# Performance work log

Hardware: AMD Instinct MI355X
Metric: run time of the kernel (lower is better)

The kernel has to match this reference:

```python
import jax, jax.numpy as jnp
import numpy as np

POOL = (7, 7)          # pool_size (Ph, Pw)
N_REGIONS = 32         # n_regions kept after IoU suppression
IOU_THR = 0.4          # IoU_threshold
B, R, H, W, C = 4, 160, 128, 128, 64


def _iou_matrix(boxes):
    # boxes: [R, 4] in (x, y, w, h); standard pairwise IoU
    x0, y0 = boxes[:, 0], boxes[:, 1]
    x1, y1 = x0 + boxes[:, 2], y0 + boxes[:, 3]
    xa = jnp.maximum(x0[:, None], x0[None, :])
    ya = jnp.maximum(y0[:, None], y0[None, :])
    xb = jnp.minimum(x1[:, None], x1[None, :])
    yb = jnp.minimum(y1[:, None], y1[None, :])
    inter = jnp.maximum(xb - xa, 0.0) * jnp.maximum(yb - ya, 0.0)
    area = boxes[:, 2] * boxes[:, 3]
    return inter / (area[:, None] + area[None, :] - inter)


def _nms_indices(boxes, thr, n_regions):
    # Greedy duplicate suppression in given (descending-objectness) order,
    # then first n_regions surviving indices, padded with the last index (R-1).
    r = boxes.shape[0]
    iou = _iou_matrix(boxes)
    ar = jnp.arange(r)

    def step(keep, i):
        sup = keep[i] & (iou[i] > thr) & (ar > i)
        return keep & ~sup, None

    keep, _ = jax.lax.scan(step, jnp.ones((r,), bool), jnp.arange(r - 1))
    rank = jnp.cumsum(keep) - 1                      # position among kept
    pos = jnp.where(keep, rank, n_regions)           # non-kept / overflow -> dropped
    idx = jnp.full((n_regions,), r - 1, dtype=jnp.int32)
    return idx.at[pos].set(ar.astype(jnp.int32), mode='drop')


def _fix_span(lo, hi, p, s):
    # enforce hi - lo >= p within [0, s], replicating clip_RoI's padding logic
    pad = p - (hi - lo)
    fmin = lo < pad // 2
    fmax = (s - hi) < (1 + pad) // 2
    sym = (pad > 0) & ~(fmin | fmax)
    lo2 = jnp.where(sym, lo - pad // 2, lo)
    hi2 = jnp.where(sym, hi + (1 + pad) // 2, hi)
    lo2 = jnp.where((pad > 0) & fmin, 0, lo2)
    hi2 = jnp.where((pad > 0) & fmin, p, hi2)
    lo2 = jnp.where((pad > 0) & fmax, s - p, lo2)
    hi2 = jnp.where((pad > 0) & fmax, s, hi2)
    return lo2, hi2


def _clip_rois(roi, h, w, ph, pw):
    x0 = jnp.maximum(0, roi[..., 0].astype(jnp.int32))
    y0 = jnp.maximum(0, roi[..., 1].astype(jnp.int32))
    x1 = jnp.minimum(w, (roi[..., 0] + roi[..., 2]).astype(jnp.int32))
    y1 = jnp.minimum(h, (roi[..., 1] + roi[..., 3]).astype(jnp.int32))
    x0, x1 = _fix_span(x0, x1, pw, w)
    y0, y1 = _fix_span(y0, y1, ph, h)
    return jnp.stack([x0, y0, x1 - x0, y1 - y0], axis=-1)  # (x, y, w, h) ints


def _pool_image(feat, boxes):
    # feat: [H, W, C]; boxes: [R, 4] int (x, y, w, h), w>=Pw, h>=Ph guaranteed
    hh, ww, _ = feat.shape
    ph, pw = POOL
    rows = jnp.arange(hh)
    cols = jnp.arange(ww)

    def pool_one(box):
        x0, y0, w_, h_ = box[0], box[1], box[2], box[3]
        hs = h_ // ph
        ws = w_ // pw
        # row-cell assignment: cell i = [i*hs, (i+1)*hs), last cell extends to h
        rseg = jnp.where((rows >= y0) & (rows < y0 + h_),
                         jnp.clip((rows - y0) // hs, 0, ph - 1), ph)
        rmax = jax.ops.segment_max(feat, rseg, num_segments=ph + 1)[:ph]  # [Ph, W, C]
        cseg = jnp.where((cols >= x0) & (cols < x0 + w_),
                         jnp.clip((cols - x0) // ws, 0, pw - 1), pw)
        cmax = jax.ops.segment_max(jnp.swapaxes(rmax, 0, 1), cseg,
                                   num_segments=pw + 1)[:pw]              # [Pw, Ph, C]
        return jnp.swapaxes(cmax, 0, 1)                                   # [Ph, Pw, C]

    return jax.vmap(pool_one)(boxes)


def setup_inputs() -> dict:
    key = jax.random.key(0)
    k1, k2, k3 = jax.random.split(key, 3)
    features = jax.random.normal(k1, (B, R and (B, H, W, C))[1] if False else (B, H, W, C), dtype=jnp.float32)
    xy = jax.random.uniform(k2, (B, R, 2), dtype=jnp.float32) * jnp.array([W - 8.0, H - 8.0], jnp.float32)
    wh = 8.0 + jax.random.uniform(k3, (B, R, 2), dtype=jnp.float32) * 56.0
    roi = jnp.concatenate([xy, wh], axis=-1)  # [B, R, 4] (x, y, w, h)
    return {"features": features, "roi": roi}


def reference(features, roi):
    b, h, w, _ = features.shape
    idx = jax.vmap(lambda bx: _nms_indices(bx, IOU_THR, N_REGIONS))(roi)     # [B, n_regions]
    pruned = jnp.take_along_axis(roi, idx[..., None], axis=1)                # [B, n_regions, 4]
    clipped = _clip_rois(pruned, h, w, POOL[0], POOL[1])                     # int boxes
    return jnp.stack([_pool_image(features[i], clipped[i]) for i in range(b)])  # [B, n_regions, Ph, Pw, C]
```

## Files before the change

kernel.cpp:

```cpp
#include <hip/hip_runtime.h>

#define BB 4
#define RR 160
#define HH 128
#define WW 128
#define CC 64
#define NREG 32
#define PH 7
#define PW 7
#define IOU_THRF 0.4f

__device__ __forceinline__ int fdiv(int a, int b) {
    int q = a / b, r = a % b;
    return (r != 0 && ((r < 0) != (b < 0))) ? q - 1 : q;
}

__device__ __forceinline__ void fix_span(int& lo, int& hi, int p, int s) {
    int pad = p - (hi - lo);
    bool fmin = lo < fdiv(pad, 2);
    bool fmax = (s - hi) < fdiv(1 + pad, 2);
    bool sym = (pad > 0) && !(fmin || fmax);
    int lo2 = sym ? lo - fdiv(pad, 2) : lo;
    int hi2 = sym ? hi + fdiv(1 + pad, 2) : hi;
    if ((pad > 0) && fmin) { lo2 = 0; hi2 = p; }
    if ((pad > 0) && fmax) { lo2 = s - p; hi2 = s; }
    lo = lo2; hi = hi2;
}

__device__ __forceinline__ float4 fmax4(float4 a, float4 b) {
    a.x = fmaxf(a.x, b.x); a.y = fmaxf(a.y, b.y);
    a.z = fmaxf(a.z, b.z); a.w = fmaxf(a.w, b.w);
    return a;
}

__device__ __forceinline__ void build_rows(int w, int tlo, int thi, int lane,
                                           const float* sx, const float* sy,
                                           const float* sx1, const float* sy1,
                                           const float* sarea,
                                           unsigned long long (*nsup)[3]) {
    const int j  = w * 64 + lane;
    const int jc = j < RR ? j : RR - 1;
    const float jx0 = sx[jc], jy0 = sy[jc], jx1 = sx1[jc], jy1 = sy1[jc], ja = sarea[jc];
    const bool jok = j < RR;

    #pragma unroll 4
    for (int t = tlo; t < thi; ++t) {
        const float xa = fmaxf(sx[t], jx0);
        const float ya = fmaxf(sy[t], jy0);
        const float xb = fminf(sx1[t], jx1);
        const float yb = fminf(sy1[t], jy1);
        const float iw  = fmaxf(__fsub_rn(xb, xa), 0.0f);
        const float ihh = fmaxf(__fsub_rn(yb, ya), 0.0f);
        const float inter = __fmul_rn(iw, ihh);
        const float denom = __fsub_rn(__fadd_rn(sarea[t], ja), inter);
        const bool pred = jok && (j > t) && (__fdiv_rn(inter, denom) > IOU_THRF);
        const unsigned long long bal = __ballot(pred);
        if (lane == 0) nsup[t][w] = ~bal;
    }
}

__global__ __launch_bounds__(1024)
void nms_clip_kernel(const float* __restrict__ roi, int* __restrict__ boxes_out) {
    const int b = blockIdx.x;
    const int tid = threadIdx.x;
    const int wid = tid >> 6;
    const int lane = tid & 63;

    __shared__ float sx[RR], sy[RR], sx1[RR], sy1[RR], sarea[RR];
    __shared__ unsigned long long nsup[RR][3];

    const float* rb = roi + (size_t)b * RR * 4;
    if (tid < RR) {
        const float4 r4 = reinterpret_cast<const float4*>(rb)[tid];
        sx[tid] = r4.x; sy[tid] = r4.y;
        sx1[tid] = __fadd_rn(r4.x, r4.z);
        sy1[tid] = __fadd_rn(r4.y, r4.w);
        sarea[tid] = __fmul_rn(r4.z, r4.w);
    }
    __syncthreads();

    {
        int w, tlo, thi;
        if (wid < 5)       { w = 0; tlo = wid * 64 / 5;               thi = (wid + 1) * 64 / 5; }
        else if (wid < 10) { w = 1; int c = wid - 5;  tlo = c * 64 / 5; thi = (c + 1) * 64 / 5; }
        else               { w = 2; int c = wid - 10; tlo = c * 64 / 6; thi = (c + 1) * 64 / 6; }
        build_rows(w, tlo, thi, lane, sx, sy, sx1, sy1, sarea, nsup);
    }
    __syncthreads();

    unsigned long long k0 = ~0ull, k1 = ~0ull, k2 = (1ull << 32) - 1;
    bool done = false;

    for (int tb = 0; tb < 64 && !done; tb += 8) {
        #pragma unroll
        for (int t0 = 0; t0 < 8; ++t0) {
            const int t = tb + t0;
            unsigned long long mb = ((k0 >> t) & 1ull) - 1ull;
            k0 &= nsup[t][0] | mb;
            k1 &= nsup[t][1] | mb;
            k2 &= nsup[t][2] | mb;
        }
        const unsigned long long pfx =
            (tb + 8 >= 64) ? ~0ull : ((1ull << (tb + 8)) - 1ull);
        if (__popcll(k0 & pfx) >= NREG) { k0 &= pfx; k1 = 0; k2 = 0; done = true; }
    }

    if (!done) {
        {
            int w, tlo;
            if (wid < 8) { w = 1; tlo = 64 + wid * 8; }
            else         { w = 2; tlo = 64 + (wid - 8) * 8; }
            build_rows(w, tlo, tlo + 8, lane, sx, sy, sx1, sy1, sarea, nsup);
        }
        __syncthreads();

        const int cnt0 = __popcll(k0);
        for (int tb = 64; tb < 128 && !done; tb += 8) {
            #pragma unroll
            for (int t0 = 0; t0 < 8; ++t0) {
                const int t = tb + t0;
                unsigned long long mb = ((k1 >> (t - 64)) & 1ull) - 1ull;
                k1 &= nsup[t][1] | mb;
                k2 &= nsup[t][2] | mb;
            }
            const unsigned long long pfx =
                (tb - 64 + 8 >= 64) ? ~0ull : ((1ull << (tb - 64 + 8)) - 1ull);
            if (cnt0 + __popcll(k1 & pfx) >= NREG) { k1 &= pfx; k2 = 0; done = true; }
        }

        if (!done) {
            {
                const int tlo = 128 + wid * 2;
                const int thi = min(tlo + 2, 159);
                if (tlo < 159)
                    build_rows(2, tlo, thi, lane, sx, sy, sx1, sy1, sarea, nsup);
            }
            __syncthreads();

            const int cnt01 = cnt0 + __popcll(k1);
            for (int tb = 128; tb < 159 && !done; tb += 8) {
                const int te = (tb + 8 < 159) ? tb + 8 : 159;
                for (int t = tb; t < te; ++t) {
                    unsigned long long mb = ((k2 >> (t - 128)) & 1ull) - 1ull;
                    k2 &= nsup[t][2] | mb;
                }
                const unsigned long long pfx =
                    ((te - 128) >= 64) ? ~0ull : ((1ull << (te - 128)) - 1ull);
                if (cnt01 + __popcll(k2 & pfx) >= NREG) { k2 &= pfx; done = true; }
            }
        }
    }

    if (tid >= NREG) return;

    int src = RR - 1;
    {
        int target = tid;
        unsigned long long words[3] = {k0, k1, k2};
        #pragma unroll
        for (int w = 0; w < 3; ++w) {
            int pc = __popcll(words[w]);
            if (target < pc) {
                unsigned long long x = words[w];
                for (int q = 0; q < target; ++q) x &= x - 1;
                src = w * 64 + (__ffsll((long long)x) - 1);
                break;
            }
            target -= pc;
        }
    }

    int x0 = max(0, (int)sx[src]);
    int y0 = max(0, (int)sy[src]);
    int x1 = min(WW, (int)sx1[src]);
    int y1 = min(HH, (int)sy1[src]);
    fix_span(x0, x1, PW, WW);
    fix_span(y0, y1, PH, HH);
    int* o = boxes_out + ((size_t)b * NREG + tid) * 4;
    o[0] = x0; o[1] = y0; o[2] = x1 - x0; o[3] = y1 - y0;
}

__global__ __launch_bounds__(PW * CC)
void pool_kernel(const float* __restrict__ feat, const int* __restrict__ boxes,
                 float* __restrict__ out) {
    const int g = blockIdx.x;
    const int x = g & 7;
    const int q = g >> 3;
    const int pair = x * 16 + q / 7;
    const int i = q % 7;
    const int n = pair & (NREG - 1);
    const int b = pair >> 5;

    const int wave = threadIdx.x >> 6;
    const int lane = threadIdx.x & 63;
    const int poff = lane >> 4;
    const int cq   = lane & 15;

    const int4 bx = *reinterpret_cast<const int4*>(boxes + ((size_t)b * NREG + n) * 4);
    const int x0 = bx.x, y0 = bx.y, w = bx.z, h = bx.w;
    const int hs = h / PH, wsz = w / PW;

    const int r0 = y0 + i * hs;
    const int r1 = (i == PH - 1) ? (y0 + h) : (r0 + hs);
    const int c0 = x0 + wave * wsz;
    const int c1 = (wave == PW - 1) ? (x0 + w) : (c0 + wsz);
    const int nr = r1 - r0;
    const int ng = (c1 - c0 + 3) >> 2;

    const float* fb = feat + (size_t)b * HH * WW * CC + (size_t)cq * 4;

    const float4 NEG = make_float4(-INFINITY, -INFINITY, -INFINITY, -INFINITY);
    float4 a0 = NEG, a1 = NEG, a2 = NEG, a3 = NEG;

    for (int gg = 0; gg < ng; ++gg) {
        int px = c0 + (gg << 2) + poff;
        px = px < c1 ? px : c1 - 1;
        const float* colp = fb + (size_t)px * CC;
        for (int rr = 0; rr < nr; rr += 4) {
            const int q1 = min(rr + 1, nr - 1);
            const int q2 = min(rr + 2, nr - 1);
            const int q3 = min(rr + 3, nr - 1);
            const float4 t0 = *reinterpret_cast<const float4*>(colp + (size_t)(r0 + rr) * (WW * CC));
            const float4 t1 = *reinterpret_cast<const float4*>(colp + (size_t)(r0 + q1) * (WW * CC));
            const float4 t2 = *reinterpret_cast<const float4*>(colp + (size_t)(r0 + q2) * (WW * CC));
            const float4 t3 = *reinterpret_cast<const float4*>(colp + (size_t)(r0 + q3) * (WW * CC));
            a0 = fmax4(a0, t0);
            a1 = fmax4(a1, t1);
            a2 = fmax4(a2, t2);
            a3 = fmax4(a3, t3);
        }
    }
    float4 v = fmax4(fmax4(a0, a1), fmax4(a2, a3));

    v.x = fmaxf(v.x, __shfl_xor(v.x, 16));
    v.y = fmaxf(v.y, __shfl_xor(v.y, 16));
    v.z = fmaxf(v.z, __shfl_xor(v.z, 16));
    v.w = fmaxf(v.w, __shfl_xor(v.w, 16));
    v.x = fmaxf(v.x, __shfl_xor(v.x, 32));
    v.y = fmaxf(v.y, __shfl_xor(v.y, 32));
    v.z = fmaxf(v.z, __shfl_xor(v.z, 32));
    v.w = fmaxf(v.w, __shfl_xor(v.w, 32));

    if (poff == 0) {
        float4* o = reinterpret_cast<float4*>(
            out + ((((size_t)b * NREG + n) * PH + i) * PW + wave) * CC) + cq;
        *o = v;
    }
}

extern "C" void kernel_launch(void* const* d_in, const int* in_sizes, int n_in,
                              void* d_out, int out_size, void* d_ws, size_t ws_size,
                              hipStream_t stream) {
    const float* features = (const float*)d_in[0];
    const float* roi      = (const float*)d_in[1];
    float* out = (float*)d_out;
    int* boxes = (int*)d_ws;

    nms_clip_kernel<<<BB, 1024, 0, stream>>>(roi, boxes);
    pool_kernel<<<BB * NREG * PH, PW * CC, 0, stream>>>(features, boxes, out);
}
```

Measured before the change: 20.77 us.

## Build suppression word 0 first and defer other words until needed

The first phase now builds only the first 64-bit suppression word for rows 0–63. Each wave handles 4 rows, so the first scan can start sooner. The other words for rows 0–127 are built only if the first 64 candidates do not yield enough survivors. The greedy scans also run in wave 0 alone, with its early-exit decision shared through a shared-memory flag. This adds extra barriers and an extra replay pass over rows 0–63 for words 1 and 2 when the fast path fails.

```diff
diff --git a/kernel.cpp b/kernel.cpp
--- a/kernel.cpp
+++ b/kernel.cpp
@@ -68,6 +68,7 @@
 
     __shared__ float sx[RR], sy[RR], sx1[RR], sy1[RR], sarea[RR];
     __shared__ unsigned long long nsup[RR][3];
+    __shared__ int sdone;
 
     const float* rb = roi + (size_t)b * RR * 4;
     if (tid < RR) {
@@ -79,56 +80,67 @@
     }
     __syncthreads();
 
-    {
-        int w, tlo, thi;
-        if (wid < 5)       { w = 0; tlo = wid * 64 / 5;               thi = (wid + 1) * 64 / 5; }
-        else if (wid < 10) { w = 1; int c = wid - 5;  tlo = c * 64 / 5; thi = (c + 1) * 64 / 5; }
-        else               { w = 2; int c = wid - 10; tlo = c * 64 / 6; thi = (c + 1) * 64 / 6; }
-        build_rows(w, tlo, thi, lane, sx, sy, sx1, sy1, sarea, nsup);
-    }
+    build_rows(0, wid * 4, wid * 4 + 4, lane, sx, sy, sx1, sy1, sarea, nsup);
     __syncthreads();
 
     unsigned long long k0 = ~0ull, k1 = ~0ull, k2 = (1ull << 32) - 1;
-    bool done = false;
-
-    for (int tb = 0; tb < 64 && !done; tb += 8) {
-        #pragma unroll
-        for (int t0 = 0; t0 < 8; ++t0) {
-            const int t = tb + t0;
-            unsigned long long mb = ((k0 >> t) & 1ull) - 1ull;
-            k0 &= nsup[t][0] | mb;
-            k1 &= nsup[t][1] | mb;
-            k2 &= nsup[t][2] | mb;
-        }
-        const unsigned long long pfx =
-            (tb + 8 >= 64) ? ~0ull : ((1ull << (tb + 8)) - 1ull);
-        if (__popcll(k0 & pfx) >= NREG) { k0 &= pfx; k1 = 0; k2 = 0; done = true; }
-    }
-
-    if (!done) {
-        {
-            int w, tlo;
-            if (wid < 8) { w = 1; tlo = 64 + wid * 8; }
-            else         { w = 2; tlo = 64 + (wid - 8) * 8; }
-            build_rows(w, tlo, tlo + 8, lane, sx, sy, sx1, sy1, sarea, nsup);
-        }
-        __syncthreads();
-
-        const int cnt0 = __popcll(k0);
-        for (int tb = 64; tb < 128 && !done; tb += 8) {
+
+    if (wid == 0) {
+        bool done = false;
+        for (int tb = 0; tb < 64 && !done; tb += 8) {
             #pragma unroll
             for (int t0 = 0; t0 < 8; ++t0) {
                 const int t = tb + t0;
-                unsigned long long mb = ((k1 >> (t - 64)) & 1ull) - 1ull;
+                unsigned long long mb = ((k0 >> t) & 1ull) - 1ull;
+                k0 &= nsup[t][0] | mb;
+            }
+            const unsigned long long pfx =
+                (tb + 8 >= 64) ? ~0ull : ((1ull << (tb + 8)) - 1ull);
+            if (__popcll(k0 & pfx) >= NREG) { k0 &= pfx; done = true; }
+        }
+        if (lane == 0) sdone = done ? 1 : 0;
+    }
+    __syncthreads();
+
+    const int d0 = sdone;
+    if (d0) {
+        k1 = 0; k2 = 0;
+    } else {
+        {
+            int w, tlo;
+            if (wid < 8) { w = 1; tlo = wid * 16; }
+            else         { w = 2; tlo = (wid - 8) * 16; }
+            build_rows(w, tlo, tlo + 16, lane, sx, sy, sx1, sy1, sarea, nsup);
+        }
+        __syncthreads();
+
+        if (wid == 0) {
+            #pragma unroll 8
+            for (int t = 0; t < 64; ++t) {
+                unsigned long long mb = ((k0 >> t) & 1ull) - 1ull;
                 k1 &= nsup[t][1] | mb;
                 k2 &= nsup[t][2] | mb;
             }
-            const unsigned long long pfx =
-                (tb - 64 + 8 >= 64) ? ~0ull : ((1ull << (tb - 64 + 8)) - 1ull);
-            if (cnt0 + __popcll(k1 & pfx) >= NREG) { k1 &= pfx; k2 = 0; done = true; }
-        }
-
-        if (!done) {
+            bool done = false;
+            const int cnt0 = __popcll(k0);
+            for (int tb = 64; tb < 128 && !done; tb += 8) {
+                #pragma unroll
+                for (int t0 = 0; t0 < 8; ++t0) {
+                    const int t = tb + t0;
+                    unsigned long long mb = ((k1 >> (t - 64)) & 1ull) - 1ull;
+                    k1 &= nsup[t][1] | mb;
+                    k2 &= nsup[t][2] | mb;
+                }
+                const unsigned long long pfx =
+                    (tb - 64 + 8 >= 64) ? ~0ull : ((1ull << (tb - 64 + 8)) - 1ull);
+                if (cnt0 + __popcll(k1 & pfx) >= NREG) { k1 &= pfx; k2 = 0; done = true; }
+            }
+            if (lane == 0) sdone = done ? 1 : 0;
+        }
+        __syncthreads();
+
+        const int d1 = sdone;
+        if (!d1) {
             {
                 const int tlo = 128 + wid * 2;
                 const int thi = min(tlo + 2, 159);
@@ -137,16 +149,19 @@
             }
             __syncthreads();
 
-            const int cnt01 = cnt0 + __popcll(k1);
-            for (int tb = 128; tb < 159 && !done; tb += 8) {
-                const int te = (tb + 8 < 159) ? tb + 8 : 159;
-                for (int t = tb; t < te; ++t) {
-                    unsigned long long mb = ((k2 >> (t - 128)) & 1ull) - 1ull;
-                    k2 &= nsup[t][2] | mb;
+            if (wid == 0) {
+                bool done = false;
+                const int cnt01 = __popcll(k0) + __popcll(k1);
+                for (int tb = 128; tb < 159 && !done; tb += 8) {
+                    const int te = (tb + 8 < 159) ? tb + 8 : 159;
+                    for (int t = tb; t < te; ++t) {
+                        unsigned long long mb = ((k2 >> (t - 128)) & 1ull) - 1ull;
+                        k2 &= nsup[t][2] | mb;
+                    }
+                    const unsigned long long pfx =
+                        ((te - 128) >= 64) ? ~0ull : ((1ull << (te - 128)) - 1ull);
+                    if (cnt01 + __popcll(k2 & pfx) >= NREG) { k2 &= pfx; done = true; }
                 }
-                const unsigned long long pfx =
-                    ((te - 128) >= 64) ? ~0ull : ((1ull << (te - 128)) - 1ull);
-                if (cnt01 + __popcll(k2 & pfx) >= NREG) { k2 &= pfx; done = true; }
             }
         }
     }
```

New measurement: 16.89 us, median of 2. -18.7%, faster.
